# Kernel optimization log

Hardware: AMD Instinct MI355X
Metric: run time of the kernel (lower is better)

The kernel has to match this reference:

```python
import jax, jax.numpy as jnp
import numpy as np

N_FEAT = 256
NUM_HEADS = 8
EPS = 1e-12  # torch F.normalize default eps


def setup_inputs() -> dict:
    key = jax.random.key(0)
    k1, k2, k3 = jax.random.split(key, 3)
    b, c, h, w = 1, N_FEAT, 64, 64
    x = jax.random.normal(k1, (b, c, h, w), dtype=jnp.float32)
    # 1x1 convs == channel GEMMs; store as (out_ch, in_ch) matrices
    w_qkv = jax.random.normal(k2, (3 * c, c), dtype=jnp.float32) * (1.0 / np.sqrt(c))
    w_proj = jax.random.normal(k3, (c, c), dtype=jnp.float32) * (1.0 / np.sqrt(c))
    temperature = jnp.ones((NUM_HEADS, 1, 1), dtype=jnp.float32)
    return {"x": x, "w_qkv": w_qkv, "w_proj": w_proj, "temperature": temperature}


def _l2norm(t):
    n = jnp.linalg.norm(t, axis=-1, keepdims=True)
    return t / jnp.maximum(n, EPS)


def reference(x, w_qkv, w_proj, temperature):
    b, c, h, w = x.shape
    heads = temperature.shape[0]
    d = c // heads
    hw = h * w
    xf = x.reshape(b, c, hw)
    # qkv 1x1 conv: (b, 3c, hw)
    qkv = jnp.einsum('oc,bcs->bos', w_qkv, xf)
    qkv = qkv.reshape(b, 3, heads, d, hw)
    q, k, v = qkv[:, 0], qkv[:, 1], qkv[:, 2]  # (b, heads, d, hw)
    q = jnp.swapaxes(q, -2, -1)  # (b, heads, hw, d)
    k = jnp.swapaxes(k, -2, -1)
    v = jnp.swapaxes(v, -2, -1)
    q = _l2norm(q)
    k = _l2norm(k)
    attn = jnp.einsum('bhsd,bhtd->bhst', q, k) * temperature[None]  # (b, heads, hw, hw)
    attn = jax.nn.softmax(attn, axis=-1)
    out = jnp.einsum('bhst,bhtd->bhsd', attn, v)  # (b, heads, hw, d)
    # faithful to torch: permute(0,2,1,3).reshape(b,c,h,w)
    out = out.transpose(0, 2, 1, 3).reshape(b, c, h, w)
    out = jnp.einsum('oc,bchw->bohw', w_proj, out)
    return out
```

## Files before the change

kernel.cpp:

```cpp
#include <hip/hip_runtime.h>
#include <stdint.h>

#define HW 4096
#define NH 8
#define NSPLIT 4
#define TSPLIT (HW / NSPLIT)

typedef __attribute__((ext_vector_type(8))) short short8;
typedef __attribute__((ext_vector_type(4))) float floatx4;

__device__ inline float bf2f(uint16_t u) {
  union { uint32_t i; float f; } v; v.i = ((uint32_t)u) << 16; return v.f;
}
__device__ inline float bflo(uint32_t u) {
  union { uint32_t i; float f; } v; v.i = u << 16; return v.f;
}
__device__ inline float bfhi(uint32_t u) {
  union { uint32_t i; float f; } v; v.i = u & 0xFFFF0000u; return v.f;
}
__device__ inline uint16_t f2bf(float f) {
  union { float f; uint32_t i; } v; v.f = f;
  uint32_t u = v.i; u += 0x7fffu + ((u >> 16) & 1u); return (uint16_t)(u >> 16);
}
__device__ inline uint32_t asu(float f) { union { float f; uint32_t i; } v; v.f = f; return v.i; }
__device__ inline uint32_t pk2r(float a, float b) {
#if __has_builtin(__builtin_amdgcn_cvt_pk_bf16_f32)
  union { short2 s; uint32_t u; } x;
  x.s = __builtin_amdgcn_cvt_pk_bf16_f32(a, b);
  return x.u;
#else
  return __builtin_amdgcn_perm(asu(b) + 0x8000u, asu(a) + 0x8000u, 0x07060302u);
#endif
}
__device__ inline short8 mk_s8(uint32_t a, uint32_t b, uint32_t c, uint32_t d) {
  union { uint32_t u[4]; short8 s; } x;
  x.u[0] = a; x.u[1] = b; x.u[2] = c; x.u[3] = d; return x.s;
}
__device__ inline bool is_f32(const uint32_t* Tp32) { return (Tp32[0] & 0xFFFFu) == 0u; }
__device__ inline float read_temp(const void* Tp, int h) {
  if (is_f32((const uint32_t*)Tp)) return ((const float*)Tp)[h];
  return bf2f(((const uint16_t*)Tp)[h]);
}

__global__ __launch_bounds__(256) void k_gemm_qkv(const void* __restrict__ X,
                                                  const void* __restrict__ A,
                                                  const void* __restrict__ Tp,
                                                  uint16_t* __restrict__ Qr,
                                                  uint16_t* __restrict__ Kr,
                                                  uint16_t* __restrict__ Vr) {
  __shared__ uint16_t sA[128 * 64];
  __shared__ uint16_t sB[32 * 64];
  __shared__ uint16_t sXr[64 * 34];
  int tid = threadIdx.x;
  int w = tid >> 6, lane = tid & 63, lm = lane & 15, qd = lane >> 4;
  int n0 = blockIdx.x * 32, m0 = blockIdx.y * 128;
  bool aF32 = is_f32((const uint32_t*)Tp);
  floatx4 acc[2][2];
#pragma unroll
  for (int i = 0; i < 2; ++i)
#pragma unroll
    for (int j = 0; j < 2; ++j) acc[i][j] = (floatx4){0.f, 0.f, 0.f, 0.f};

  for (int k0 = 0; k0 < 256; k0 += 64) {
    __syncthreads();
    {
      int cl = tid >> 2, sc = (tid & 3) * 8;
      uint32_t* l32 = (uint32_t*)sXr;
      int base = cl * 17 + (sc >> 1);
      if (aF32) {
        const float4* x4 = (const float4*)((const float*)X + (k0 + cl) * HW + n0 + sc);
        float4 a = x4[0], b = x4[1];
        l32[base + 0] = pk2r(a.x, a.y); l32[base + 1] = pk2r(a.z, a.w);
        l32[base + 2] = pk2r(b.x, b.y); l32[base + 3] = pk2r(b.z, b.w);
      } else {
        uint4 a = *(const uint4*)((const uint16_t*)X + (k0 + cl) * HW + n0 + sc);
        l32[base + 0] = a.x; l32[base + 1] = a.y;
        l32[base + 2] = a.z; l32[base + 3] = a.w;
      }
    }
#pragma unroll
    for (int r = 0; r < 4; ++r) {
      int ch = r * 256 + tid; int row = ch >> 3, c8 = ch & 7;
      uint4 v;
      if (aF32) {
        const float4* s4 = (const float4*)((const float*)A + (m0 + row) * 256 + k0 + c8 * 8);
        float4 a = s4[0], b = s4[1];
        v = make_uint4(pk2r(a.x, a.y), pk2r(a.z, a.w), pk2r(b.x, b.y), pk2r(b.z, b.w));
      } else {
        v = *(const uint4*)((const uint16_t*)A + (m0 + row) * 256 + k0 + c8 * 8);
      }
      *(uint4*)(&sA[row * 64 + (c8 ^ (row & 7)) * 8]) = v;
    }
    __syncthreads();
    {
      int sl = tid >> 3, cs = (tid & 7) * 8;
      uint32_t wb[4];
#pragma unroll
      for (int j = 0; j < 4; ++j) {
        uint32_t lo = sXr[(cs + 2 * j) * 34 + sl];
        uint32_t hi = sXr[(cs + 2 * j + 1) * 34 + sl];
        wb[j] = lo | (hi << 16);
      }
      *(uint4*)(&sB[sl * 64 + (((cs >> 3) ^ (sl & 7))) * 8]) =
          make_uint4(wb[0], wb[1], wb[2], wb[3]);
    }
    __syncthreads();
#pragma unroll
    for (int kk = 0; kk < 2; ++kk) {
      short8 af[2];
#pragma unroll
      for (int mt = 0; mt < 2; ++mt) {
        int row = w * 32 + mt * 16 + lm;
        af[mt] = *(const short8*)(&sA[row * 64 + ((kk * 4 + qd) ^ (row & 7)) * 8]);
      }
#pragma unroll
      for (int nt = 0; nt < 2; ++nt) {
        int row = nt * 16 + lm;
        short8 bf = *(const short8*)(&sB[row * 64 + ((kk * 4 + qd) ^ (row & 7)) * 8]);
#pragma unroll
        for (int mt = 0; mt < 2; ++mt)
          acc[mt][nt] = __builtin_amdgcn_mfma_f32_16x16x32_bf16(af[mt], bf, acc[mt][nt], 0, 0, 0);
      }
    }
  }
  int ow = m0 + w * 32;
  int type = ow >> 8;
  int hh = (ow >> 5) & 7;
  float tv = read_temp(Tp, hh);
#pragma unroll
  for (int nt = 0; nt < 2; ++nt) {
    int s = n0 + nt * 16 + lm;
    if (type < 2) {
      float ssq = 0.f;
#pragma unroll
      for (int mt = 0; mt < 2; ++mt)
#pragma unroll
        for (int r = 0; r < 4; ++r) ssq += acc[mt][nt][r] * acc[mt][nt][r];
      ssq += __shfl_xor(ssq, 16, 64);
      ssq += __shfl_xor(ssq, 32, 64);
      float sc = (type == 0 ? tv * 1.44269504088896340736f : 1.0f) /
                 fmaxf(sqrtf(ssq), 1e-12f);
      uint16_t* dst = (type == 0 ? Qr : Kr) + ((hh << 12) + s) * 32;
#pragma unroll
      for (int mt = 0; mt < 2; ++mt)
        *(uint2*)(dst + mt * 16 + qd * 4) =
            make_uint2(pk2r(acc[mt][nt][0] * sc, acc[mt][nt][1] * sc),
                       pk2r(acc[mt][nt][2] * sc, acc[mt][nt][3] * sc));
    } else {
#pragma unroll
      for (int mt = 0; mt < 2; ++mt)
#pragma unroll
        for (int r = 0; r < 4; ++r)
          Vr[(hh * 32 + mt * 16 + qd * 4 + r) * HW + s] = f2bf(acc[mt][nt][r]);
    }
  }
}

__global__ __launch_bounds__(256, 4) void k_attn(const uint16_t* __restrict__ Qr,
                                                 const uint16_t* __restrict__ Kr,
                                                 const uint16_t* __restrict__ Vr,
                                                 const void* __restrict__ Tp,
                                                 uint16_t* __restrict__ Op,
                                                 float* __restrict__ Lp) {
  __shared__ uint16_t sK[256 * 32];
  __shared__ uint16_t sV[32 * 256];
  int tid = threadIdx.x;
  int w = tid >> 6, lane = tid & 63, lm = lane & 15, qd = lane >> 4;
  int bid = blockIdx.x;
  int h = bid & 7;
  int j = bid >> 3;
  int sp = j & 3;
  int qb = j >> 2;
  int srow = qb * 128 + w * 32;
  const float c1 = 1.44269504088896340736f;
  float c2 = fabsf(read_temp(Tp, h)) * c1;
  short8 qf0 = *(const short8*)(Qr + ((h << 12) + srow + lm) * 32 + qd * 8);
  short8 qf1 = *(const short8*)(Qr + ((h << 12) + srow + 16 + lm) * 32 + qd * 8);
  const uint16_t* Kg = Kr + (h << 12) * 32;
  const uint16_t* Vg = Vr + (h * 32) * HW;
  floatx4 o00 = {0.f, 0.f, 0.f, 0.f}, o01 = {0.f, 0.f, 0.f, 0.f};
  floatx4 o10 = {0.f, 0.f, 0.f, 0.f}, o11 = {0.f, 0.f, 0.f, 0.f};
  floatx4 l0 = {0.f, 0.f, 0.f, 0.f}, l1 = {0.f, 0.f, 0.f, 0.f};
  const short8 ones8 = mk_s8(0x3F803F80u, 0x3F803F80u, 0x3F803F80u, 0x3F803F80u);
  const floatx4 zb = {-c2, -c2, -c2, -c2};
  const int kswz = (qd ^ ((lm >> 1) & 3)) * 8;

  int rK = tid >> 2, cK = tid & 3;
  uint16_t* dk0 = &sK[rK * 32 + (cK ^ ((rK >> 1) & 3)) * 8];
  const uint16_t* gk0 = Kg + (sp * TSPLIT + rK) * 32 + cK * 8;
  int dVb = tid >> 5, cVx = tid & 31;
  int s0x = dVb >> 1;
  bool sw = dVb & 1;
  uint16_t* dv0 = &sV[dVb * 256 + (cVx ^ s0x) * 8];
  uint16_t* dv1 = &sV[(dVb + 8) * 256 + (cVx ^ s0x ^ 4) * 8];
  const uint16_t* gv0 = Vg + dVb * HW + sp * TSPLIT + cVx * 8;

  uint4 rk0 = *(const uint4*)gk0;
  uint4 rk1 = *(const uint4*)(gk0 + 2048);
  uint4 rk2 = *(const uint4*)(gk0 + 4096);
  uint4 rk3 = *(const uint4*)(gk0 + 6144);
  uint4 rv0 = *(const uint4*)gv0;
  uint4 rv1 = *(const uint4*)(gv0 + 8 * HW);
  uint4 rv2 = *(const uint4*)(gv0 + 16 * HW);
  uint4 rv3 = *(const uint4*)(gv0 + 24 * HW);

  for (int i = 0; i < TSPLIT / 256; ++i) {
    __syncthreads();
    *(uint4*)dk0 = rk0;
    *(uint4*)(dk0 + 2048) = rk1;
    *(uint4*)(dk0 + 4096) = rk2;
    *(uint4*)(dk0 + 6144) = rk3;
    *(uint4*)dv0 = sw ? make_uint4(rv0.z, rv0.w, rv0.x, rv0.y) : rv0;
    *(uint4*)(dv0 + 4096) = sw ? make_uint4(rv2.z, rv2.w, rv2.x, rv2.y) : rv2;
    *(uint4*)dv1 = sw ? make_uint4(rv1.z, rv1.w, rv1.x, rv1.y) : rv1;
    *(uint4*)(dv1 + 4096) = sw ? make_uint4(rv3.z, rv3.w, rv3.x, rv3.y) : rv3;
    if (i + 1 < TSPLIT / 256) {
      gk0 += 256 * 32; gv0 += 256;
      rk0 = *(const uint4*)gk0;
      rk1 = *(const uint4*)(gk0 + 2048);
      rk2 = *(const uint4*)(gk0 + 4096);
      rk3 = *(const uint4*)(gk0 + 6144);
      rv0 = *(const uint4*)gv0;
      rv1 = *(const uint4*)(gv0 + 8 * HW);
      rv2 = *(const uint4*)(gv0 + 16 * HW);
      rv3 = *(const uint4*)(gv0 + 24 * HW);
    }
    asm volatile("s_waitcnt lgkmcnt(0)\n\ts_barrier" ::: "memory");
#pragma unroll
    for (int nt = 0; nt < 8; ++nt) {
      short8 kfa = *(const short8*)(&sK[(nt * 32 + lm) * 32 + kswz]);
      short8 kfb = *(const short8*)(&sK[(nt * 32 + 16 + lm) * 32 + kswz]);
      int gpa = (nt * 8 + qd) ^ lm;
      int gpb = (nt * 8 + 4 + qd) ^ lm;
      uint2 va0 = *(const uint2*)(&sV[lm * 256 + gpa * 4]);
      uint2 vb0 = *(const uint2*)(&sV[lm * 256 + gpb * 4]);
      uint2 va1 = *(const uint2*)(&sV[(lm + 16) * 256 + gpa * 4]);
      uint2 vb1 = *(const uint2*)(&sV[(lm + 16) * 256 + gpb * 4]);
      short8 vv0 = mk_s8(va0.x, va0.y, vb0.x, vb0.y);
      short8 vv1 = mk_s8(va1.x, va1.y, vb1.x, vb1.y);
      floatx4 sa = __builtin_amdgcn_mfma_f32_16x16x32_bf16(kfa, qf0, zb, 0, 0, 0);
      floatx4 sb = __builtin_amdgcn_mfma_f32_16x16x32_bf16(kfb, qf0, zb, 0, 0, 0);
      short8 pa = mk_s8(
          pk2r(__builtin_amdgcn_exp2f(sa[0]), __builtin_amdgcn_exp2f(sa[1])),
          pk2r(__builtin_amdgcn_exp2f(sa[2]), __builtin_amdgcn_exp2f(sa[3])),
          pk2r(__builtin_amdgcn_exp2f(sb[0]), __builtin_amdgcn_exp2f(sb[1])),
          pk2r(__builtin_amdgcn_exp2f(sb[2]), __builtin_amdgcn_exp2f(sb[3])));
      o00 = __builtin_amdgcn_mfma_f32_16x16x32_bf16(pa, vv0, o00, 0, 0, 0);
      o01 = __builtin_amdgcn_mfma_f32_16x16x32_bf16(pa, vv1, o01, 0, 0, 0);
      l0  = __builtin_amdgcn_mfma_f32_16x16x32_bf16(pa, ones8, l0, 0, 0, 0);
      sa = __builtin_amdgcn_mfma_f32_16x16x32_bf16(kfa, qf1, zb, 0, 0, 0);
      sb = __builtin_amdgcn_mfma_f32_16x16x32_bf16(kfb, qf1, zb, 0, 0, 0);
      pa = mk_s8(
          pk2r(__builtin_amdgcn_exp2f(sa[0]), __builtin_amdgcn_exp2f(sa[1])),
          pk2r(__builtin_amdgcn_exp2f(sa[2]), __builtin_amdgcn_exp2f(sa[3])),
          pk2r(__builtin_amdgcn_exp2f(sb[0]), __builtin_amdgcn_exp2f(sb[1])),
          pk2r(__builtin_amdgcn_exp2f(sb[2]), __builtin_amdgcn_exp2f(sb[3])));
      o10 = __builtin_amdgcn_mfma_f32_16x16x32_bf16(pa, vv0, o10, 0, 0, 0);
      o11 = __builtin_amdgcn_mfma_f32_16x16x32_bf16(pa, vv1, o11, 0, 0, 0);
      l1  = __builtin_amdgcn_mfma_f32_16x16x32_bf16(pa, ones8, l1, 0, 0, 0);
    }
  }
  int sb_ = (sp * NH + h) * HW + srow;
  uint16_t* op = Op + (size_t)sb_ * 32;
#pragma unroll
  for (int r = 0; r < 4; ++r) {
    op[(qd * 4 + r) * 32 + lm] = f2bf(o00[r]);
    op[(qd * 4 + r) * 32 + 16 + lm] = f2bf(o01[r]);
    op[(16 * 32) + (qd * 4 + r) * 32 + lm] = f2bf(o10[r]);
    op[(16 * 32) + (qd * 4 + r) * 32 + 16 + lm] = f2bf(o11[r]);
  }
  if (lm == 0) {
#pragma unroll
    for (int r = 0; r < 4; ++r) {
      Lp[sb_ + qd * 4 + r] = l0[r];
      Lp[sb_ + 16 + qd * 4 + r] = l1[r];
    }
  }
}

__global__ __launch_bounds__(256) void k_gemm_proj(const void* __restrict__ A,
                                                   const uint16_t* __restrict__ Op,
                                                   const float* __restrict__ Lp,
                                                   void* __restrict__ C,
                                                   const uint32_t* __restrict__ Tp32) {
  __shared__ uint16_t sA[64 * 64];
  __shared__ uint16_t sB[32 * 64];
  __shared__ float sOp[64 * 33];
  int tid = threadIdx.x;
  int w = tid >> 6, lane = tid & 63, lm = lane & 15, qd = lane >> 4;
  int n0 = blockIdx.x * 32, m0 = blockIdx.y * 64;
  int h = (n0 >> 5) & 7, slo = n0 >> 8;
  bool aF32 = is_f32(Tp32);
  floatx4 acc[2];
  acc[0] = (floatx4){0.f, 0.f, 0.f, 0.f};
  acc[1] = (floatx4){0.f, 0.f, 0.f, 0.f};
  int cl = tid >> 2, dp = (tid & 3) * 8;
  int dd = tid >> 3, spart = (tid & 7) * 8;

  for (int k0 = 0; k0 < 256; k0 += 64) {
    __syncthreads();
#pragma unroll
    for (int r = 0; r < 2; ++r) {
      int ch = r * 256 + tid; int row = ch >> 3, c8 = ch & 7;
      uint4 v;
      if (aF32) {
        const float4* s4 = (const float4*)((const float*)A + (m0 + row) * 256 + k0 + c8 * 8);
        float4 a = s4[0], b = s4[1];
        v = make_uint4(pk2r(a.x, a.y), pk2r(a.z, a.w), pk2r(b.x, b.y), pk2r(b.z, b.w));
      } else {
        v = *(const uint4*)((const uint16_t*)A + (m0 + row) * 256 + k0 + c8 * 8);
      }
      *(uint4*)(&sA[row * 64 + (c8 ^ (row & 7)) * 8]) = v;
    }
    {
      int s = slo + 16 * (k0 + cl);
      float L = 0.f;
      float a[8];
#pragma unroll
      for (int q = 0; q < 8; ++q) a[q] = 0.f;
#pragma unroll
      for (int sp = 0; sp < NSPLIT; ++sp) {
        size_t gj = (size_t)(sp * NH + h) * HW + s;
        L += Lp[gj];
        uint4 x = *(const uint4*)(Op + gj * 32 + dp);
        a[0] += bflo(x.x); a[1] += bfhi(x.x); a[2] += bflo(x.y); a[3] += bfhi(x.y);
        a[4] += bflo(x.z); a[5] += bfhi(x.z); a[6] += bflo(x.w); a[7] += bfhi(x.w);
      }
      float inv = __builtin_amdgcn_rcpf(L);
#pragma unroll
      for (int q = 0; q < 8; ++q) sOp[cl * 33 + dp + q] = a[q] * inv;
    }
    __syncthreads();
    {
      float b[8];
#pragma unroll
      for (int q = 0; q < 8; ++q) b[q] = sOp[(spart + q) * 33 + dd];
      *(uint4*)(&sB[dd * 64 + ((spart >> 3) ^ (dd & 7)) * 8]) =
          make_uint4(pk2r(b[0], b[1]), pk2r(b[2], b[3]),
                     pk2r(b[4], b[5]), pk2r(b[6], b[7]));
    }
    __syncthreads();
#pragma unroll
    for (int kk = 0; kk < 2; ++kk) {
      int arow = w * 16 + lm;
      short8 af = *(const short8*)(&sA[arow * 64 + ((kk * 4 + qd) ^ (arow & 7)) * 8]);
#pragma unroll
      for (int nt = 0; nt < 2; ++nt) {
        int row = nt * 16 + lm;
        short8 bf = *(const short8*)(&sB[row * 64 + ((kk * 4 + qd) ^ (row & 7)) * 8]);
        acc[nt] = __builtin_amdgcn_mfma_f32_16x16x32_bf16(af, bf, acc[nt], 0, 0, 0);
      }
    }
  }
  bool f32o = is_f32(Tp32);
#pragma unroll
  for (int nt = 0; nt < 2; ++nt)
#pragma unroll
    for (int r = 0; r < 4; ++r) {
      int row = m0 + w * 16 + qd * 4 + r;
      int col = n0 + nt * 16 + lm;
      if (f32o) ((float*)C)[row * HW + col] = acc[nt][r];
      else ((uint16_t*)C)[row * HW + col] = f2bf(acc[nt][r]);
    }
}

extern "C" void kernel_launch(void* const* d_in, const int* in_sizes, int n_in,
                              void* d_out, int out_size, void* d_ws, size_t ws_size,
                              hipStream_t stream) {
  const void* X  = d_in[0];
  const void* Wq = d_in[1];
  const void* Wp = d_in[2];
  const void* Tp = d_in[3];
  const uint32_t* Tp32 = (const uint32_t*)Tp;
  uint16_t* ws = (uint16_t*)d_ws;
  uint16_t* Qr = ws;
  uint16_t* Kr = Qr + NH * HW * 32;
  uint16_t* Vr = Kr + NH * HW * 32;
  uint16_t* Op = Vr + NH * 32 * HW;
  float* Lp = (float*)(Op + (size_t)NSPLIT * NH * HW * 32);

  k_gemm_qkv<<<dim3(128, 6), 256, 0, stream>>>(X, Wq, Tp, Qr, Kr, Vr);
  k_attn<<<dim3(1024), 256, 0, stream>>>(Qr, Kr, Vr, Tp, Op, Lp);
  k_gemm_proj<<<dim3(128, 4), 256, 0, stream>>>(Wp, Op, Lp, d_out, Tp32);
}
```

Measured before the change: 109.6 us.

## Load GEMM weight fragments directly to registers and double-buffer X tile

```diff
diff --git a/kernel.cpp b/kernel.cpp
--- a/kernel.cpp
+++ b/kernel.cpp
@@ -48,9 +48,7 @@
                                                   uint16_t* __restrict__ Qr,
                                                   uint16_t* __restrict__ Kr,
                                                   uint16_t* __restrict__ Vr) {
-  __shared__ uint16_t sA[128 * 64];
-  __shared__ uint16_t sB[32 * 64];
-  __shared__ uint16_t sXr[64 * 34];
+  __shared__ uint16_t sB[2][32 * 64];
   int tid = threadIdx.x;
   int w = tid >> 6, lane = tid & 63, lm = lane & 15, qd = lane >> 4;
   int n0 = blockIdx.x * 32, m0 = blockIdx.y * 128;
@@ -61,67 +59,87 @@
 #pragma unroll
     for (int j = 0; j < 2; ++j) acc[i][j] = (floatx4){0.f, 0.f, 0.f, 0.f};
 
-  for (int k0 = 0; k0 < 256; k0 += 64) {
+  int xs = tid & 31, xc8 = tid >> 5;
+  const float* Xf = (const float*)X + (size_t)xc8 * 8 * HW + n0 + xs;
+  const uint16_t* Xh = (const uint16_t*)X + (size_t)xc8 * 8 * HW + n0 + xs;
+  const float* Af = (const float*)A;
+  const uint16_t* Ah = (const uint16_t*)A;
+  int wr0 = (m0 + w * 32 + lm) * 256;
+  int wr1 = (m0 + w * 32 + 16 + lm) * 256;
+
+  float xr[8];
+  uint32_t xhh[8];
+  if (aF32) {
+#pragma unroll
+    for (int jj = 0; jj < 8; ++jj) xr[jj] = Xf[jj * HW];
+  } else {
+#pragma unroll
+    for (int jj = 0; jj < 8; ++jj) xhh[jj] = Xh[jj * HW];
+  }
+
+  int wswz = xs * 64 + (xc8 ^ (xs & 7)) * 8;
+  int cur = 0;
+  for (int ks = 0; ks < 4; ++ks) {
+    int k0 = ks * 64;
+    {
+      uint32_t xw0, xw1, xw2, xw3;
+      if (aF32) {
+        xw0 = pk2r(xr[0], xr[1]); xw1 = pk2r(xr[2], xr[3]);
+        xw2 = pk2r(xr[4], xr[5]); xw3 = pk2r(xr[6], xr[7]);
+      } else {
+        xw0 = xhh[0] | (xhh[1] << 16); xw1 = xhh[2] | (xhh[3] << 16);
+        xw2 = xhh[4] | (xhh[5] << 16); xw3 = xhh[6] | (xhh[7] << 16);
+      }
+      *(uint4*)(&sB[cur][wswz]) = make_uint4(xw0, xw1, xw2, xw3);
+    }
+    short8 af[2][2];
+    float4 wf[2][2][2];
+    if (aF32) {
+#pragma unroll
+      for (int mt = 0; mt < 2; ++mt)
+#pragma unroll
+        for (int kk = 0; kk < 2; ++kk) {
+          const float4* p = (const float4*)(Af + (mt ? wr1 : wr0) + k0 + (kk * 4 + qd) * 8);
+          wf[mt][kk][0] = p[0]; wf[mt][kk][1] = p[1];
+        }
+    } else {
+#pragma unroll
+      for (int mt = 0; mt < 2; ++mt)
+#pragma unroll
+        for (int kk = 0; kk < 2; ++kk)
+          af[mt][kk] = *(const short8*)(Ah + (mt ? wr1 : wr0) + k0 + (kk * 4 + qd) * 8);
+    }
     __syncthreads();
-    {
-      int cl = tid >> 2, sc = (tid & 3) * 8;
-      uint32_t* l32 = (uint32_t*)sXr;
-      int base = cl * 17 + (sc >> 1);
+    if (ks < 3) {
       if (aF32) {
-        const float4* x4 = (const float4*)((const float*)X + (k0 + cl) * HW + n0 + sc);
-        float4 a = x4[0], b = x4[1];
-        l32[base + 0] = pk2r(a.x, a.y); l32[base + 1] = pk2r(a.z, a.w);
-        l32[base + 2] = pk2r(b.x, b.y); l32[base + 3] = pk2r(b.z, b.w);
+#pragma unroll
+        for (int jj = 0; jj < 8; ++jj) xr[jj] = Xf[(k0 + 64 + jj) * HW];
       } else {
-        uint4 a = *(const uint4*)((const uint16_t*)X + (k0 + cl) * HW + n0 + sc);
-        l32[base + 0] = a.x; l32[base + 1] = a.y;
-        l32[base + 2] = a.z; l32[base + 3] = a.w;
-      }
-    }
-#pragma unroll
-    for (int r = 0; r < 4; ++r) {
-      int ch = r * 256 + tid; int row = ch >> 3, c8 = ch & 7;
-      uint4 v;
-      if (aF32) {
-        const float4* s4 = (const float4*)((const float*)A + (m0 + row) * 256 + k0 + c8 * 8);
-        float4 a = s4[0], b = s4[1];
-        v = make_uint4(pk2r(a.x, a.y), pk2r(a.z, a.w), pk2r(b.x, b.y), pk2r(b.z, b.w));
-      } else {
-        v = *(const uint4*)((const uint16_t*)A + (m0 + row) * 256 + k0 + c8 * 8);
-      }
-      *(uint4*)(&sA[row * 64 + (c8 ^ (row & 7)) * 8]) = v;
-    }
-    __syncthreads();
-    {
-      int sl = tid >> 3, cs = (tid & 7) * 8;
-      uint32_t wb[4];
-#pragma unroll
-      for (int j = 0; j < 4; ++j) {
-        uint32_t lo = sXr[(cs + 2 * j) * 34 + sl];
-        uint32_t hi = sXr[(cs + 2 * j + 1) * 34 + sl];
-        wb[j] = lo | (hi << 16);
-      }
-      *(uint4*)(&sB[sl * 64 + (((cs >> 3) ^ (sl & 7))) * 8]) =
-          make_uint4(wb[0], wb[1], wb[2], wb[3]);
-    }
-    __syncthreads();
-#pragma unroll
-    for (int kk = 0; kk < 2; ++kk) {
-      short8 af[2];
-#pragma unroll
-      for (int mt = 0; mt < 2; ++mt) {
-        int row = w * 32 + mt * 16 + lm;
-        af[mt] = *(const short8*)(&sA[row * 64 + ((kk * 4 + qd) ^ (row & 7)) * 8]);
-      }
+#pragma unroll
+        for (int jj = 0; jj < 8; ++jj) xhh[jj] = Xh[(k0 + 64 + jj) * HW];
+      }
+    }
+    if (aF32) {
+#pragma unroll
+      for (int mt = 0; mt < 2; ++mt)
+#pragma unroll
+        for (int kk = 0; kk < 2; ++kk) {
+          float4 a = wf[mt][kk][0], b = wf[mt][kk][1];
+          af[mt][kk] = mk_s8(pk2r(a.x, a.y), pk2r(a.z, a.w),
+                             pk2r(b.x, b.y), pk2r(b.z, b.w));
+        }
+    }
+#pragma unroll
+    for (int kk = 0; kk < 2; ++kk)
 #pragma unroll
       for (int nt = 0; nt < 2; ++nt) {
-        int row = nt * 16 + lm;
-        short8 bf = *(const short8*)(&sB[row * 64 + ((kk * 4 + qd) ^ (row & 7)) * 8]);
+        short8 bf = *(const short8*)(&sB[cur][(nt * 16 + lm) * 64 +
+                                             ((kk * 4 + qd) ^ (lm & 7)) * 8]);
 #pragma unroll
         for (int mt = 0; mt < 2; ++mt)
-          acc[mt][nt] = __builtin_amdgcn_mfma_f32_16x16x32_bf16(af[mt], bf, acc[mt][nt], 0, 0, 0);
-      }
-    }
+          acc[mt][nt] = __builtin_amdgcn_mfma_f32_16x16x32_bf16(af[mt][kk], bf, acc[mt][nt], 0, 0, 0);
+      }
+    cur ^= 1;
   }
   int ow = m0 + w * 32;
   int type = ow >> 8;
@@ -283,7 +301,6 @@
                                                    const float* __restrict__ Lp,
                                                    void* __restrict__ C,
                                                    const uint32_t* __restrict__ Tp32) {
-  __shared__ uint16_t sA[64 * 64];
   __shared__ uint16_t sB[32 * 64];
   __shared__ float sOp[64 * 33];
   int tid = threadIdx.x;
@@ -291,6 +308,9 @@
   int n0 = blockIdx.x * 32, m0 = blockIdx.y * 64;
   int h = (n0 >> 5) & 7, slo = n0 >> 8;
   bool aF32 = is_f32(Tp32);
+  const float* Af = (const float*)A;
+  const uint16_t* Ah = (const uint16_t*)A;
+  int wr = (m0 + w * 16 + lm) * 256;
   floatx4 acc[2];
   acc[0] = (floatx4){0.f, 0.f, 0.f, 0.f};
   acc[1] = (floatx4){0.f, 0.f, 0.f, 0.f};
@@ -298,35 +318,35 @@
   int dd = tid >> 3, spart = (tid & 7) * 8;
 
   for (int k0 = 0; k0 < 256; k0 += 64) {
+    short8 af[2];
+    float4 wf[2][2];
+    if (aF32) {
+#pragma unroll
+      for (int kk = 0; kk < 2; ++kk) {
+        const float4* p = (const float4*)(Af + wr + k0 + (kk * 4 + qd) * 8);
+        wf[kk][0] = p[0]; wf[kk][1] = p[1];
+      }
+    } else {
+#pragma unroll
+      for (int kk = 0; kk < 2; ++kk)
+        af[kk] = *(const short8*)(Ah + wr + k0 + (kk * 4 + qd) * 8);
+    }
+    int s = slo + 16 * (k0 + cl);
+    float L = 0.f;
+    float a[8];
+#pragma unroll
+    for (int q = 0; q < 8; ++q) a[q] = 0.f;
+#pragma unroll
+    for (int sp = 0; sp < NSPLIT; ++sp) {
+      size_t gj = (size_t)(sp * NH + h) * HW + s;
+      L += Lp[gj];
+      uint4 x = *(const uint4*)(Op + gj * 32 + dp);
+      a[0] += bflo(x.x); a[1] += bfhi(x.x); a[2] += bflo(x.y); a[3] += bfhi(x.y);
+      a[4] += bflo(x.z); a[5] += bfhi(x.z); a[6] += bflo(x.w); a[7] += bfhi(x.w);
+    }
+    float inv = __builtin_amdgcn_rcpf(L);
     __syncthreads();
-#pragma unroll
-    for (int r = 0; r < 2; ++r) {
-      int ch = r * 256 + tid; int row = ch >> 3, c8 = ch & 7;
-      uint4 v;
-      if (aF32) {
-        const float4* s4 = (const float4*)((const float*)A + (m0 + row) * 256 + k0 + c8 * 8);
-        float4 a = s4[0], b = s4[1];
-        v = make_uint4(pk2r(a.x, a.y), pk2r(a.z, a.w), pk2r(b.x, b.y), pk2r(b.z, b.w));
-      } else {
-        v = *(const uint4*)((const uint16_t*)A + (m0 + row) * 256 + k0 + c8 * 8);
-      }
-      *(uint4*)(&sA[row * 64 + (c8 ^ (row & 7)) * 8]) = v;
-    }
     {
-      int s = slo + 16 * (k0 + cl);
-      float L = 0.f;
-      float a[8];
-#pragma unroll
-      for (int q = 0; q < 8; ++q) a[q] = 0.f;
-#pragma unroll
-      for (int sp = 0; sp < NSPLIT; ++sp) {
-        size_t gj = (size_t)(sp * NH + h) * HW + s;
-        L += Lp[gj];
-        uint4 x = *(const uint4*)(Op + gj * 32 + dp);
-        a[0] += bflo(x.x); a[1] += bfhi(x.x); a[2] += bflo(x.y); a[3] += bfhi(x.y);
-        a[4] += bflo(x.z); a[5] += bfhi(x.z); a[6] += bflo(x.w); a[7] += bfhi(x.w);
-      }
-      float inv = __builtin_amdgcn_rcpf(L);
 #pragma unroll
       for (int q = 0; q < 8; ++q) sOp[cl * 33 + dp + q] = a[q] * inv;
     }
@@ -340,17 +360,21 @@
                      pk2r(b[4], b[5]), pk2r(b[6], b[7]));
     }
     __syncthreads();
-#pragma unroll
-    for (int kk = 0; kk < 2; ++kk) {
-      int arow = w * 16 + lm;
-      short8 af = *(const short8*)(&sA[arow * 64 + ((kk * 4 + qd) ^ (arow & 7)) * 8]);
+    if (aF32) {
+#pragma unroll
+      for (int kk = 0; kk < 2; ++kk) {
+        float4 x = wf[kk][0], y = wf[kk][1];
+        af[kk] = mk_s8(pk2r(x.x, x.y), pk2r(x.z, x.w), pk2r(y.x, y.y), pk2r(y.z, y.w));
+      }
+    }
+#pragma unroll
+    for (int kk = 0; kk < 2; ++kk)
 #pragma unroll
       for (int nt = 0; nt < 2; ++nt) {
         int row = nt * 16 + lm;
         short8 bf = *(const short8*)(&sB[row * 64 + ((kk * 4 + qd) ^ (row & 7)) * 8]);
-        acc[nt] = __builtin_amdgcn_mfma_f32_16x16x32_bf16(af, bf, acc[nt], 0, 0, 0);
-      }
-    }
+        acc[nt] = __builtin_amdgcn_mfma_f32_16x16x32_bf16(af[kk], bf, acc[nt], 0, 0, 0);
+      }
   }
   bool f32o = is_f32(Tp32);
 #pragma unroll
```

New measurement: 113.7 us. +3.7%, slower.

## Double-buffer shared memory and prefetch next K-tile in QKV and projection GEMMs

Applied to the files above, without the earlier changes.

```diff
diff --git a/kernel.cpp b/kernel.cpp
--- a/kernel.cpp
+++ b/kernel.cpp
@@ -42,15 +42,15 @@
   return bf2f(((const uint16_t*)Tp)[h]);
 }
 
-__global__ __launch_bounds__(256) void k_gemm_qkv(const void* __restrict__ X,
-                                                  const void* __restrict__ A,
-                                                  const void* __restrict__ Tp,
-                                                  uint16_t* __restrict__ Qr,
-                                                  uint16_t* __restrict__ Kr,
-                                                  uint16_t* __restrict__ Vr) {
-  __shared__ uint16_t sA[128 * 64];
-  __shared__ uint16_t sB[32 * 64];
-  __shared__ uint16_t sXr[64 * 34];
+__global__ __launch_bounds__(256, 3) void k_gemm_qkv(const void* __restrict__ X,
+                                                     const void* __restrict__ A,
+                                                     const void* __restrict__ Tp,
+                                                     uint16_t* __restrict__ Qr,
+                                                     uint16_t* __restrict__ Kr,
+                                                     uint16_t* __restrict__ Vr) {
+  __shared__ uint16_t sA[2][128 * 64];
+  __shared__ uint16_t sB[2][32 * 64];
+  __shared__ uint16_t sXr[2][64 * 34];
   int tid = threadIdx.x;
   int w = tid >> 6, lane = tid & 63, lm = lane & 15, qd = lane >> 4;
   int n0 = blockIdx.x * 32, m0 = blockIdx.y * 128;
@@ -61,35 +61,65 @@
 #pragma unroll
     for (int j = 0; j < 2; ++j) acc[i][j] = (floatx4){0.f, 0.f, 0.f, 0.f};
 
-  for (int k0 = 0; k0 < 256; k0 += 64) {
-    __syncthreads();
+  int cl = tid >> 2, sc = (tid & 3) * 8;
+  int arow0 = tid >> 3, ac8 = tid & 7;
+
+  float4 xfa, xfb; uint4 xua;
+  float4 wfa[4][2]; uint4 wua[4];
+
+#define QKV_LOADX(K0)                                                          \
+  do {                                                                         \
+    if (aF32) {                                                                \
+      const float4* x4 = (const float4*)((const float*)X + ((K0) + cl) * HW + n0 + sc); \
+      xfa = x4[0]; xfb = x4[1];                                                \
+    } else {                                                                   \
+      xua = *(const uint4*)((const uint16_t*)X + ((K0) + cl) * HW + n0 + sc);  \
+    }                                                                          \
+  } while (0)
+#define QKV_LOADW(K0)                                                          \
+  do {                                                                         \
+    _Pragma("unroll") for (int r = 0; r < 4; ++r) {                            \
+      int row = r * 32 + arow0;                                                \
+      if (aF32) {                                                              \
+        const float4* s4 = (const float4*)((const float*)A + (m0 + row) * 256 + (K0) + ac8 * 8); \
+        wfa[r][0] = s4[0]; wfa[r][1] = s4[1];                                  \
+      } else {                                                                 \
+        wua[r] = *(const uint4*)((const uint16_t*)A + (m0 + row) * 256 + (K0) + ac8 * 8); \
+      }                                                                        \
+    }                                                                          \
+  } while (0)
+
+  QKV_LOADX(0);
+  QKV_LOADW(0);
+  int cur = 0;
+  for (int ks = 0; ks < 4; ++ks) {
+    int k0 = ks * 64;
     {
-      int cl = tid >> 2, sc = (tid & 3) * 8;
-      uint32_t* l32 = (uint32_t*)sXr;
+      uint32_t* l32 = (uint32_t*)sXr[cur];
       int base = cl * 17 + (sc >> 1);
       if (aF32) {
-        const float4* x4 = (const float4*)((const float*)X + (k0 + cl) * HW + n0 + sc);
-        float4 a = x4[0], b = x4[1];
-        l32[base + 0] = pk2r(a.x, a.y); l32[base + 1] = pk2r(a.z, a.w);
-        l32[base + 2] = pk2r(b.x, b.y); l32[base + 3] = pk2r(b.z, b.w);
+        l32[base + 0] = pk2r(xfa.x, xfa.y); l32[base + 1] = pk2r(xfa.z, xfa.w);
+        l32[base + 2] = pk2r(xfb.x, xfb.y); l32[base + 3] = pk2r(xfb.z, xfb.w);
       } else {
-        uint4 a = *(const uint4*)((const uint16_t*)X + (k0 + cl) * HW + n0 + sc);
-        l32[base + 0] = a.x; l32[base + 1] = a.y;
-        l32[base + 2] = a.z; l32[base + 3] = a.w;
+        l32[base + 0] = xua.x; l32[base + 1] = xua.y;
+        l32[base + 2] = xua.z; l32[base + 3] = xua.w;
       }
     }
 #pragma unroll
     for (int r = 0; r < 4; ++r) {
-      int ch = r * 256 + tid; int row = ch >> 3, c8 = ch & 7;
+      int row = r * 32 + arow0;
       uint4 v;
       if (aF32) {
-        const float4* s4 = (const float4*)((const float*)A + (m0 + row) * 256 + k0 + c8 * 8);
-        float4 a = s4[0], b = s4[1];
+        float4 a = wfa[r][0], b = wfa[r][1];
         v = make_uint4(pk2r(a.x, a.y), pk2r(a.z, a.w), pk2r(b.x, b.y), pk2r(b.z, b.w));
       } else {
-        v = *(const uint4*)((const uint16_t*)A + (m0 + row) * 256 + k0 + c8 * 8);
-      }
-      *(uint4*)(&sA[row * 64 + (c8 ^ (row & 7)) * 8]) = v;
+        v = wua[r];
+      }
+      *(uint4*)(&sA[cur][row * 64 + (ac8 ^ (row & 7)) * 8]) = v;
+    }
+    if (ks < 3) {
+      QKV_LOADX(k0 + 64);
+      QKV_LOADW(k0 + 64);
     }
     __syncthreads();
     {
@@ -97,11 +127,11 @@
       uint32_t wb[4];
 #pragma unroll
       for (int j = 0; j < 4; ++j) {
-        uint32_t lo = sXr[(cs + 2 * j) * 34 + sl];
-        uint32_t hi = sXr[(cs + 2 * j + 1) * 34 + sl];
+        uint32_t lo = sXr[cur][(cs + 2 * j) * 34 + sl];
+        uint32_t hi = sXr[cur][(cs + 2 * j + 1) * 34 + sl];
         wb[j] = lo | (hi << 16);
       }
-      *(uint4*)(&sB[sl * 64 + (((cs >> 3) ^ (sl & 7))) * 8]) =
+      *(uint4*)(&sB[cur][sl * 64 + (((cs >> 3) ^ (sl & 7))) * 8]) =
           make_uint4(wb[0], wb[1], wb[2], wb[3]);
     }
     __syncthreads();
@@ -111,18 +141,21 @@
 #pragma unroll
       for (int mt = 0; mt < 2; ++mt) {
         int row = w * 32 + mt * 16 + lm;
-        af[mt] = *(const short8*)(&sA[row * 64 + ((kk * 4 + qd) ^ (row & 7)) * 8]);
+        af[mt] = *(const short8*)(&sA[cur][row * 64 + ((kk * 4 + qd) ^ (row & 7)) * 8]);
       }
 #pragma unroll
       for (int nt = 0; nt < 2; ++nt) {
         int row = nt * 16 + lm;
-        short8 bf = *(const short8*)(&sB[row * 64 + ((kk * 4 + qd) ^ (row & 7)) * 8]);
+        short8 bf = *(const short8*)(&sB[cur][row * 64 + ((kk * 4 + qd) ^ (row & 7)) * 8]);
 #pragma unroll
         for (int mt = 0; mt < 2; ++mt)
           acc[mt][nt] = __builtin_amdgcn_mfma_f32_16x16x32_bf16(af[mt], bf, acc[mt][nt], 0, 0, 0);
       }
     }
-  }
+    cur ^= 1;
+  }
+#undef QKV_LOADX
+#undef QKV_LOADW
   int ow = m0 + w * 32;
   int type = ow >> 8;
   int hh = (ow >> 5) & 7;
@@ -138,14 +171,14 @@
         for (int r = 0; r < 4; ++r) ssq += acc[mt][nt][r] * acc[mt][nt][r];
       ssq += __shfl_xor(ssq, 16, 64);
       ssq += __shfl_xor(ssq, 32, 64);
-      float sc = (type == 0 ? tv * 1.44269504088896340736f : 1.0f) /
-                 fmaxf(sqrtf(ssq), 1e-12f);
+      float sc2 = (type == 0 ? tv * 1.44269504088896340736f : 1.0f) /
+                  fmaxf(sqrtf(ssq), 1e-12f);
       uint16_t* dst = (type == 0 ? Qr : Kr) + ((hh << 12) + s) * 32;
 #pragma unroll
       for (int mt = 0; mt < 2; ++mt)
         *(uint2*)(dst + mt * 16 + qd * 4) =
-            make_uint2(pk2r(acc[mt][nt][0] * sc, acc[mt][nt][1] * sc),
-                       pk2r(acc[mt][nt][2] * sc, acc[mt][nt][3] * sc));
+            make_uint2(pk2r(acc[mt][nt][0] * sc2, acc[mt][nt][1] * sc2),
+                       pk2r(acc[mt][nt][2] * sc2, acc[mt][nt][3] * sc2));
     } else {
 #pragma unroll
       for (int mt = 0; mt < 2; ++mt)
@@ -278,14 +311,14 @@
   }
 }
 
-__global__ __launch_bounds__(256) void k_gemm_proj(const void* __restrict__ A,
-                                                   const uint16_t* __restrict__ Op,
-                                                   const float* __restrict__ Lp,
-                                                   void* __restrict__ C,
-                                                   const uint32_t* __restrict__ Tp32) {
-  __shared__ uint16_t sA[64 * 64];
-  __shared__ uint16_t sB[32 * 64];
-  __shared__ float sOp[64 * 33];
+__global__ __launch_bounds__(256, 2) void k_gemm_proj(const void* __restrict__ A,
+                                                      const uint16_t* __restrict__ Op,
+                                                      const float* __restrict__ Lp,
+                                                      void* __restrict__ C,
+                                                      const uint32_t* __restrict__ Tp32) {
+  __shared__ uint16_t sA[2][64 * 64];
+  __shared__ uint16_t sB[2][32 * 64];
+  __shared__ float sOp[2][64 * 33];
   int tid = threadIdx.x;
   int w = tid >> 6, lane = tid & 63, lm = lane & 15, qd = lane >> 4;
   int n0 = blockIdx.x * 32, m0 = blockIdx.y * 64;
@@ -296,46 +329,75 @@
   acc[1] = (floatx4){0.f, 0.f, 0.f, 0.f};
   int cl = tid >> 2, dp = (tid & 3) * 8;
   int dd = tid >> 3, spart = (tid & 7) * 8;
-
+  int arow0 = tid >> 3, ac8 = tid & 7;
+
+  uint4 ga[NSPLIT]; float glp[NSPLIT];
+  float4 wfa[2][2]; uint4 wua[2];
+
+#define PRJ_LOADG(K0)                                                          \
+  do {                                                                         \
+    int s = slo + 16 * ((K0) + cl);                                            \
+    _Pragma("unroll") for (int sp = 0; sp < NSPLIT; ++sp) {                    \
+      size_t gj = (size_t)(sp * NH + h) * HW + s;                              \
+      glp[sp] = Lp[gj];                                                        \
+      ga[sp] = *(const uint4*)(Op + gj * 32 + dp);                             \
+    }                                                                          \
+  } while (0)
+#define PRJ_LOADW(K0)                                                          \
+  do {                                                                         \
+    _Pragma("unroll") for (int r = 0; r < 2; ++r) {                            \
+      int row = r * 32 + arow0;                                                \
+      if (aF32) {                                                              \
+        const float4* s4 = (const float4*)((const float*)A + (m0 + row) * 256 + (K0) + ac8 * 8); \
+        wfa[r][0] = s4[0]; wfa[r][1] = s4[1];                                  \
+      } else {                                                                 \
+        wua[r] = *(const uint4*)((const uint16_t*)A + (m0 + row) * 256 + (K0) + ac8 * 8); \
+      }                                                                        \
+    }                                                                          \
+  } while (0)
+
+  PRJ_LOADG(0);
+  PRJ_LOADW(0);
+  int cur = 0;
   for (int k0 = 0; k0 < 256; k0 += 64) {
-    __syncthreads();
+    {
+      float L = 0.f;
+      float a[8];
+#pragma unroll
+      for (int q = 0; q < 8; ++q) a[q] = 0.f;
+#pragma unroll
+      for (int sp = 0; sp < NSPLIT; ++sp) {
+        L += glp[sp];
+        uint4 x = ga[sp];
+        a[0] += bflo(x.x); a[1] += bfhi(x.x); a[2] += bflo(x.y); a[3] += bfhi(x.y);
+        a[4] += bflo(x.z); a[5] += bfhi(x.z); a[6] += bflo(x.w); a[7] += bfhi(x.w);
+      }
+      float inv = __builtin_amdgcn_rcpf(L);
+#pragma unroll
+      for (int q = 0; q < 8; ++q) sOp[cur][cl * 33 + dp + q] = a[q] * inv;
+    }
 #pragma unroll
     for (int r = 0; r < 2; ++r) {
-      int ch = r * 256 + tid; int row = ch >> 3, c8 = ch & 7;
+      int row = r * 32 + arow0;
       uint4 v;
       if (aF32) {
-        const float4* s4 = (const float4*)((const float*)A + (m0 + row) * 256 + k0 + c8 * 8);
-        float4 a = s4[0], b = s4[1];
+        float4 a = wfa[r][0], b = wfa[r][1];
         v = make_uint4(pk2r(a.x, a.y), pk2r(a.z, a.w), pk2r(b.x, b.y), pk2r(b.z, b.w));
       } else {
-        v = *(const uint4*)((const uint16_t*)A + (m0 + row) * 256 + k0 + c8 * 8);
-      }
-      *(uint4*)(&sA[row * 64 + (c8 ^ (row & 7)) * 8]) = v;
-    }
-    {
-      int s = slo + 16 * (k0 + cl);
-      float L = 0.f;
-      float a[8];
-#pragma unroll
-      for (int q = 0; q < 8; ++q) a[q] = 0.f;
-#pragma unroll
-      for (int sp = 0; sp < NSPLIT; ++sp) {
-        size_t gj = (size_t)(sp * NH + h) * HW + s;
-        L += Lp[gj];
-        uint4 x = *(const uint4*)(Op + gj * 32 + dp);
-        a[0] += bflo(x.x); a[1] += bfhi(x.x); a[2] += bflo(x.y); a[3] += bfhi(x.y);
-        a[4] += bflo(x.z); a[5] += bfhi(x.z); a[6] += bflo(x.w); a[7] += bfhi(x.w);
-      }
-      float inv = __builtin_amdgcn_rcpf(L);
-#pragma unroll
-      for (int q = 0; q < 8; ++q) sOp[cl * 33 + dp + q] = a[q] * inv;
+        v = wua[r];
+      }
+      *(uint4*)(&sA[cur][row * 64 + (ac8 ^ (row & 7)) * 8]) = v;
+    }
+    if (k0 < 192) {
+      PRJ_LOADG(k0 + 64);
+      PRJ_LOADW(k0 + 64);
     }
     __syncthreads();
     {
       float b[8];
 #pragma unroll
-      for (int q = 0; q < 8; ++q) b[q] = sOp[(spart + q) * 33 + dd];
-      *(uint4*)(&sB[dd * 64 + ((spart >> 3) ^ (dd & 7)) * 8]) =
+      for (int q = 0; q < 8; ++q) b[q] = sOp[cur][(spart + q) * 33 + dd];
+      *(uint4*)(&sB[cur][dd * 64 + ((spart >> 3) ^ (dd & 7)) * 8]) =
           make_uint4(pk2r(b[0], b[1]), pk2r(b[2], b[3]),
                      pk2r(b[4], b[5]), pk2r(b[6], b[7]));
     }
@@ -343,15 +405,18 @@
 #pragma unroll
     for (int kk = 0; kk < 2; ++kk) {
       int arow = w * 16 + lm;
-      short8 af = *(const short8*)(&sA[arow * 64 + ((kk * 4 + qd) ^ (arow & 7)) * 8]);
+      short8 af = *(const short8*)(&sA[cur][arow * 64 + ((kk * 4 + qd) ^ (arow & 7)) * 8]);
 #pragma unroll
       for (int nt = 0; nt < 2; ++nt) {
         int row = nt * 16 + lm;
-        short8 bf = *(const short8*)(&sB[row * 64 + ((kk * 4 + qd) ^ (row & 7)) * 8]);
+        short8 bf = *(const short8*)(&sB[cur][row * 64 + ((kk * 4 + qd) ^ (row & 7)) * 8]);
         acc[nt] = __builtin_amdgcn_mfma_f32_16x16x32_bf16(af, bf, acc[nt], 0, 0, 0);
       }
     }
-  }
+    cur ^= 1;
+  }
+#undef PRJ_LOADG
+#undef PRJ_LOADW
   bool f32o = is_f32(Tp32);
 #pragma unroll
   for (int nt = 0; nt < 2; ++nt)
```

New measurement: 105.9 us. 1.04x faster.
